# Optimization experiments

Hardware: AMD Instinct MI355X
Metric: run time of the kernel (lower is better)

Reference implementation:

```python
import jax, jax.numpy as jnp
import numpy as np

BETA = 0.25          # commitment loss weight (init kwarg)
CODEBOOK_SIZE = 2048


def setup_inputs() -> dict:
    key = jax.random.key(0)
    k1, k2 = jax.random.split(key)
    B, L, D = 8, 4096, 256
    z_e = jax.random.normal(k1, (B, L, D), dtype=jnp.float32)
    # xavier_uniform-style init for the codebook
    limit = float(np.sqrt(6.0 / (CODEBOOK_SIZE + D)))
    embed_weight = jax.random.uniform(k2, (CODEBOOK_SIZE, D), dtype=jnp.float32,
                                      minval=-limit, maxval=limit)
    return {"z_e": z_e, "embed_weight": embed_weight}


def reference(z_e, embed_weight):
    # eval-mode forward (no EMA buffer updates)
    B, L, D = z_e.shape
    K = embed_weight.shape[0]
    zf = z_e.reshape(-1, D)                                   # [N, D]
    d2 = (jnp.sum(zf * zf, axis=1, keepdims=True)
          - 2.0 * (zf @ embed_weight.T)
          + jnp.sum(embed_weight * embed_weight, axis=1)[None, :])
    distances = jnp.sqrt(jnp.maximum(d2, 0.0))                # [N, K]
    idx = jnp.argmin(distances, axis=1)                       # [N]
    z_q = embed_weight[idx].reshape(B, L, D)                  # gather

    commitment_loss = BETA * jnp.mean((jax.lax.stop_gradient(z_q) - z_e) ** 2)
    embedding_loss = jnp.mean((jax.lax.stop_gradient(z_e) - z_q) ** 2)

    # avg over one-hot encodings == normalized histogram of idx
    N = zf.shape[0]
    counts = jax.ops.segment_sum(jnp.ones((N,), jnp.float32), idx, num_segments=K)
    avg_probs = counts / N
    perplexity = jnp.exp(-jnp.sum(avg_probs * jnp.log(avg_probs + 1e-10)))
    vq_loss = commitment_loss + embedding_loss - 0.01 * perplexity

    z_q_st = z_e + jax.lax.stop_gradient(z_q - z_e)           # straight-through
    return z_q_st, vq_loss, idx.reshape(B, L)
```

## Files before the change

### kernel.cpp

```cpp
#include <hip/hip_runtime.h>
#include <math.h>

#define DDIM 256
#define NSPLIT 2
#define TILES_PER_SPLIT 32
#define TILE_CODES 32
#define TILE_BYTES 16384
#define ROWS_PER_BLOCK 128

typedef __attribute__((ext_vector_type(8))) short short8v;
typedef __attribute__((ext_vector_type(4))) float float4v;
typedef unsigned int u32;
typedef unsigned short u16;

__device__ __forceinline__ short f2bf(float x) {
    u32 u = __float_as_uint(x);
    u = u + 0x7fffu + ((u >> 16) & 1u);
    return (short)(u >> 16);
}

__device__ __forceinline__ float np_sq_chain(const float* v, int lane) {
    #pragma clang fp contract(off)
    const int half = lane >> 3, j = lane & 7;
    const float* base = v + half * 128 + j;
    float x = base[0];
    float c = x * x;
    #pragma unroll
    for (int m = 1; m < 16; ++m) {
        float y = base[8 * m];
        float s = y * y;
        c = c + s;
    }
    return c;
}

__device__ __forceinline__ float np_combine16(const float* c) {
    #pragma clang fp contract(off)
    float L = ((c[0] + c[1]) + (c[2] + c[3])) + ((c[4] + c[5]) + (c[6] + c[7]));
    float R = ((c[8] + c[9]) + (c[10] + c[11])) + ((c[12] + c[13]) + (c[14] + c[15]));
    return L + R;
}

__device__ __forceinline__ void ins3(float m, int k,
                                     float& v0, float& v1, float& v2,
                                     int& i0, int& i1, int& i2) {
    if (m < v0)      { v2 = v1; i2 = i1; v1 = v0; i1 = i0; v0 = m; i0 = k; }
    else if (m < v1) { v2 = v1; i2 = i1; v1 = m;  i1 = k; }
    else if (m < v2) { v2 = m;  i2 = k; }
}

__global__ void code_norms_np_kernel(const float* __restrict__ e, float* __restrict__ e2,
                                     int* __restrict__ counts) {
    __shared__ float buf[DDIM];
    __shared__ float ch[16];
    int k = blockIdx.x;
    int t = threadIdx.x;
    if (t == 0) counts[k] = 0;
    float4 v = *(const float4*)&e[(size_t)k * DDIM + t * 4];
    *(float4*)&buf[t * 4] = v;
    __syncthreads();
    if (t < 16) ch[t] = np_sq_chain(buf, t);
    __syncthreads();
    if (t == 0) e2[k] = np_combine16(ch);
}

__global__ void convert_permute_e_kernel(const float* __restrict__ e, char* __restrict__ ebf_p) {
    int id = blockIdx.x * 256 + threadIdx.x;
    int k = id >> 5, d8 = id & 31;
    const float* s = &e[(size_t)k * DDIM + d8 * 8];
    float4 f0 = *(const float4*)s;
    float4 f1 = *(const float4*)(s + 4);
    short8v v;
    v[0] = f2bf(f0.x); v[1] = f2bf(f0.y); v[2] = f2bf(f0.z); v[3] = f2bf(f0.w);
    v[4] = f2bf(f1.x); v[5] = f2bf(f1.y); v[6] = f2bf(f1.z); v[7] = f2bf(f1.w);
    *(short8v*)(ebf_p + ((size_t)(k >> 5) << 14) + d8 * 512 + (k & 31) * 16) = v;
}

__global__ __attribute__((amdgpu_flat_work_group_size(512, 512)))
void vq_cand_kernel(const float* __restrict__ z, const char* __restrict__ ebf_p,
                    const float* __restrict__ e2, float* __restrict__ cand_v,
                    u16* __restrict__ cand_i, int N) {
    __shared__ float e2s[1024];
    const int t    = threadIdx.x;
    const int w    = t >> 6;
    const int lane = t & 63;
    const int quad = lane >> 4;
    const int l15  = lane & 15;
    const int s    = blockIdx.y;
    const int rw   = blockIdx.x * ROWS_PER_BLOCK + w * 16;

    e2s[t]       = e2[s * 1024 + t];
    e2s[t + 512] = e2[s * 1024 + 512 + t];

    short8v zf[8];
    {
        const float* zr = &z[(size_t)(rw + l15) * DDIM];
        #pragma unroll
        for (int kk = 0; kk < 8; ++kk) {
            int d0 = kk * 32 + quad * 8;
            float4 f0 = *(const float4*)&zr[d0];
            float4 f1 = *(const float4*)&zr[d0 + 4];
            short8v v;
            v[0] = f2bf(f0.x); v[1] = f2bf(f0.y); v[2] = f2bf(f0.z); v[3] = f2bf(f0.w);
            v[4] = f2bf(f1.x); v[5] = f2bf(f1.y); v[6] = f2bf(f1.z); v[7] = f2bf(f1.w);
            zf[kk] = v;
        }
    }

    __syncthreads();

    float v0 = 3.4e38f, v1 = 3.4e38f, v2 = 3.4e38f;
    int   i0 = 0x7fff,  i1 = 0x7fff,  i2 = 0x7fff;

    const char* sbase = ebf_p + (size_t)s * TILES_PER_SPLIT * TILE_BYTES
                      + quad * 512 + l15 * 16;

    #pragma unroll 1
    for (int tt = 0; tt < TILES_PER_SPLIT; ++tt) {
        const char* tg = sbase + (size_t)tt * TILE_BYTES;

        float4v acc0 = (float4v)0.0f, acc1 = (float4v)0.0f;

        #pragma unroll
        for (int kk = 0; kk < 8; ++kk) {
            short8v a0 = *(const short8v*)(tg + kk * 2048);
            short8v a1 = *(const short8v*)(tg + kk * 2048 + 256);
            acc0 = __builtin_amdgcn_mfma_f32_16x16x32_bf16(a0, zf[kk], acc0, 0, 0, 0);
            acc1 = __builtin_amdgcn_mfma_f32_16x16x32_bf16(a1, zf[kk], acc1, 0, 0, 0);
        }

        const int kloc  = tt * TILE_CODES;
        const int kbase = s * 1024 + kloc;
        float4 e2a = *(const float4*)&e2s[kloc + quad * 4];
        float4 e2b = *(const float4*)&e2s[kloc + 16 + quad * 4];
        float m;
        m = fmaf(-2.0f, acc0[0], e2a.x); ins3(m, kbase + quad * 4 + 0,      v0, v1, v2, i0, i1, i2);
        m = fmaf(-2.0f, acc1[0], e2b.x); ins3(m, kbase + 16 + quad * 4 + 0, v0, v1, v2, i0, i1, i2);
        m = fmaf(-2.0f, acc0[1], e2a.y); ins3(m, kbase + quad * 4 + 1,      v0, v1, v2, i0, i1, i2);
        m = fmaf(-2.0f, acc1[1], e2b.y); ins3(m, kbase + 16 + quad * 4 + 1, v0, v1, v2, i0, i1, i2);
        m = fmaf(-2.0f, acc0[2], e2a.z); ins3(m, kbase + quad * 4 + 2,      v0, v1, v2, i0, i1, i2);
        m = fmaf(-2.0f, acc1[2], e2b.z); ins3(m, kbase + 16 + quad * 4 + 2, v0, v1, v2, i0, i1, i2);
        m = fmaf(-2.0f, acc0[3], e2a.w); ins3(m, kbase + quad * 4 + 3,      v0, v1, v2, i0, i1, i2);
        m = fmaf(-2.0f, acc1[3], e2b.w); ins3(m, kbase + 16 + quad * 4 + 3, v0, v1, v2, i0, i1, i2);
    }

    {
        float bm0 = 3.4e38f, bm1 = 3.4e38f, bm2 = 3.4e38f;
        int   bk0 = 0x7fff,  bk1 = 0x7fff,  bk2 = 0x7fff;
        #pragma unroll
        for (int q = 0; q < 4; ++q) {
            int src = l15 + q * 16;
            float m0 = __shfl(v0, src); int k0 = __shfl(i0, src);
            float m1 = __shfl(v1, src); int k1 = __shfl(i1, src);
            float m2 = __shfl(v2, src); int k2 = __shfl(i2, src);
            ins3(m0, k0, bm0, bm1, bm2, bk0, bk1, bk2);
            ins3(m1, k1, bm0, bm1, bm2, bk0, bk1, bk2);
            ins3(m2, k2, bm0, bm1, bm2, bk0, bk1, bk2);
        }
        if (quad == 0) {
            size_t base = ((size_t)s * N + (rw + l15)) * 3;
            cand_v[base]     = bm0;  cand_i[base]     = (u16)bk0;
            cand_v[base + 1] = bm1;  cand_i[base + 1] = (u16)bk1;
            cand_v[base + 2] = bm2;  cand_i[base + 2] = (u16)bk2;
        }
    }
}

__global__ void refine_fused_kernel(const float* __restrict__ z, const float* __restrict__ e,
                                    const float* __restrict__ e2np,
                                    const float* __restrict__ cand_v,
                                    const u16* __restrict__ cand_i,
                                    int* __restrict__ counts, float* __restrict__ partials,
                                    float* __restrict__ out_zq, float* __restrict__ out_idx,
                                    int N) {
    __shared__ float buf[4][DDIM];
    __shared__ float ch[4][16];
    __shared__ float wsum[4];
    const int w = threadIdx.x >> 6;
    const int t = threadIdx.x & 63;
    const int n = blockIdx.x * 4 + w;

    float4 zv = *(const float4*)&z[(size_t)n * DDIM + t * 4];
    *(float4*)&buf[w][t * 4] = zv;
    __syncthreads();
    if (t < 16) ch[w][t] = np_sq_chain(buf[w], t);
    __syncthreads();

    float bv[6]; int bi[6];
    #pragma unroll
    for (int c = 0; c < 6; ++c) { bv[c] = 3.4e38f; bi[c] = 0x7fffffff; }
    #pragma unroll
    for (int c = 0; c < 6; ++c) {
        int sp = c / 3, j = c - sp * 3;
        size_t off = ((size_t)sp * N + n) * 3 + j;
        float v  = cand_v[off];
        int   id = (int)cand_i[off];
        #pragma unroll
        for (int x = 0; x < 6; ++x) {
            if (v < bv[x] || (v == bv[x] && id < bi[x])) {
                for (int d = 5; d > x; --d) { bv[d] = bv[d - 1]; bi[d] = bi[d - 1]; }
                bv[x] = v; bi[x] = id;
                break;
            }
        }
    }

    float dotf[6];
    #pragma unroll
    for (int c = 0; c < 6; ++c) {
        int k = bi[c];
        float4 ev = *(const float4*)&e[(size_t)k * DDIM + t * 4];
        double p = (double)zv.x * (double)ev.x + (double)zv.y * (double)ev.y
                 + (double)zv.z * (double)ev.z + (double)zv.w * (double)ev.w;
        #pragma unroll
        for (int o = 32; o > 0; o >>= 1) p += __shfl_down(p, o);
        dotf[c] = (float)p;
    }

    int bk = 0;
    if (t == 0) {
        #pragma clang fp contract(off)
        float sx = np_combine16(ch[w]);
        float bd = 3.4e38f;
        bk = 0x7fffffff;
        #pragma unroll
        for (int c = 0; c < 6; ++c) {
            float twod = 2.0f * dotf[c];
            float t1 = sx - twod;
            float d2v = t1 + e2np[bi[c]];
            d2v = fmaxf(d2v, 0.0f);
            float d = sqrtf(d2v);
            if (d < bd || (d == bd && bi[c] < bk)) { bd = d; bk = bi[c]; }
        }
    }
    int wk = __shfl(bk, 0);

    float4 ev = *(const float4*)&e[(size_t)wk * DDIM + t * 4];
    *(float4*)&out_zq[(size_t)n * DDIM + t * 4] = ev;
    float dx = zv.x - ev.x, dy = zv.y - ev.y, dz = zv.z - ev.z, dw = zv.w - ev.w;
    float sq = dx * dx + dy * dy + dz * dz + dw * dw;
    #pragma unroll
    for (int o = 32; o > 0; o >>= 1) sq += __shfl_down(sq, o);
    if (t == 0) {
        wsum[w] = sq;
        atomicAdd(&counts[wk], 1);
        out_idx[n] = (float)wk;
    }
    __syncthreads();
    if (threadIdx.x == 0)
        partials[blockIdx.x] = wsum[0] + wsum[1] + wsum[2] + wsum[3];
}

__global__ void finalize_kernel(const int* __restrict__ counts, const float* __restrict__ partials,
                                float* __restrict__ out_loss, int K, int NB,
                                float invN, float invND) {
    int t = threadIdx.x;
    double ent = 0.0, sq = 0.0;
    for (int k = t; k < K; k += 256) {
        float p = (float)counts[k] * invN;
        ent += (double)(p * logf(p + 1e-10f));
    }
    for (int i = t; i < NB; i += 256) sq += (double)partials[i];
    #pragma unroll
    for (int o = 32; o > 0; o >>= 1) {
        ent += __shfl_down(ent, o);
        sq  += __shfl_down(sq, o);
    }
    __shared__ double e4[4], s4[4];
    if ((t & 63) == 0) { e4[t >> 6] = ent; s4[t >> 6] = sq; }
    __syncthreads();
    if (t == 0) {
        double esum = e4[0] + e4[1] + e4[2] + e4[3];
        double ssum = s4[0] + s4[1] + s4[2] + s4[3];
        float perp = expf((float)(-esum));
        float mean = (float)ssum * invND;
        out_loss[0] = 1.25f * mean - 0.01f * perp;
    }
}

extern "C" void kernel_launch(void* const* d_in, const int* in_sizes, int n_in,
                              void* d_out, int out_size, void* d_ws, size_t ws_size,
                              hipStream_t stream) {
    const float* z = (const float*)d_in[0];
    const float* e = (const float*)d_in[1];
    const int N = in_sizes[0] / DDIM;
    const int K = in_sizes[1] / DDIM;

    float* out      = (float*)d_out;
    float* out_zq   = out;
    float* out_loss = out + (size_t)N * DDIM;
    float* out_idx  = out_loss + 1;

    int*   counts   = (int*)d_ws;
    float* e2np     = (float*)((char*)d_ws + 8192);
    float* partials = (float*)((char*)d_ws + 16384);
    float* cand_v   = (float*)((char*)d_ws + 49152);
    u16*   cand_i   = (u16*)((char*)d_ws + 835584);
    char*  ebf_p    = (char*)d_ws + 1228800;

    code_norms_np_kernel<<<K, 64, 0, stream>>>(e, e2np, counts);
    convert_permute_e_kernel<<<K * 32 / 256, 256, 0, stream>>>(e, ebf_p);
    vq_cand_kernel<<<dim3(N / ROWS_PER_BLOCK, NSPLIT), 512, 0, stream>>>(z, ebf_p, e2np,
                                                                         cand_v, cand_i, N);
    refine_fused_kernel<<<N / 4, 256, 0, stream>>>(z, e, e2np, cand_v, cand_i,
                                                   counts, partials, out_zq, out_idx, N);
    finalize_kernel<<<1, 256, 0, stream>>>(counts, partials, out_loss, K, N / 4,
                                           1.0f / (float)N, 1.0f / (float)(N * DDIM));
}
```

Baseline: 404.4 us.

## Stage codebook panels in LDS with double-buffered async loads and 2x4 MFMA tiles

The candidate-search kernel now converts a block's 128 z rows to bf16 into LDS and streams 64-code codebook panels into a double-buffered LDS area using global_load_lds, instead of having every wave read the codebook straight from global memory. Each of the 4 waves computes a 32-row by 64-code tile (8 MFMAs per k-step), so each A and B fragment is reused twice or four times. The aim is to cut redundant global and L2 traffic for the codebook and overlap its loads with MFMA work. In exchange it uses about 100KB of LDS and 256 threads, which limits the GPU to one block per CU and depends on vmcnt-based waits for correctness.

```diff
diff --git a/kernel.cpp b/kernel.cpp
--- a/kernel.cpp
+++ b/kernel.cpp
@@ -3,9 +3,11 @@
 
 #define DDIM 256
 #define NSPLIT 2
-#define TILES_PER_SPLIT 32
-#define TILE_CODES 32
-#define TILE_BYTES 16384
+#define SPLIT_CODES 1024
+#define SPLIT_BYTES (SPLIT_CODES * DDIM * 2)
+#define PANEL_CODES 64
+#define PANELS_PER_SPLIT 16
+#define PANEL_BYTES 32768
 #define ROWS_PER_BLOCK 128
 
 typedef __attribute__((ext_vector_type(8))) short short8v;
@@ -17,6 +19,12 @@
     u32 u = __float_as_uint(x);
     u = u + 0x7fffu + ((u >> 16) & 1u);
     return (short)(u >> 16);
+}
+
+__device__ __forceinline__ void gload_lds16(const void* g, void* l) {
+    __builtin_amdgcn_global_load_lds(
+        (const __attribute__((address_space(1))) u32*)g,
+        (__attribute__((address_space(3))) u32*)l, 16, 0, 0);
 }
 
 __device__ __forceinline__ float np_sq_chain(const float* v, int lane) {
@@ -76,10 +84,12 @@
     *(short8v*)(ebf_p + ((size_t)(k >> 5) << 14) + d8 * 512 + (k & 31) * 16) = v;
 }
 
-__global__ __attribute__((amdgpu_flat_work_group_size(512, 512)))
+__global__ __launch_bounds__(256, 1)
 void vq_cand_kernel(const float* __restrict__ z, const char* __restrict__ ebf_p,
                     const float* __restrict__ e2, float* __restrict__ cand_v,
                     u16* __restrict__ cand_i, int N) {
+    __shared__ __align__(16) char cpan[2][PANEL_BYTES];
+    __shared__ __align__(16) char zlds[65536];
     __shared__ float e2s[1024];
     const int t    = threadIdx.x;
     const int w    = t >> 6;
@@ -87,83 +97,138 @@
     const int quad = lane >> 4;
     const int l15  = lane & 15;
     const int s    = blockIdx.y;
-    const int rw   = blockIdx.x * ROWS_PER_BLOCK + w * 16;
-
+    const int rw0  = blockIdx.x * ROWS_PER_BLOCK;
+
+    const char* cbase = ebf_p + (size_t)s * SPLIT_BYTES;
+
+    #pragma unroll
+    for (int i = 0; i < 16; ++i) {
+        int u = t + i * 256;
+        int row = u >> 5, c = u & 31;
+        const float* src = &z[(size_t)(rw0 + row) * DDIM + c * 8];
+        float4 f0 = *(const float4*)src;
+        float4 f1 = *(const float4*)(src + 4);
+        short8v v;
+        v[0] = f2bf(f0.x); v[1] = f2bf(f0.y); v[2] = f2bf(f0.z); v[3] = f2bf(f0.w);
+        v[4] = f2bf(f1.x); v[5] = f2bf(f1.y); v[6] = f2bf(f1.z); v[7] = f2bf(f1.w);
+        *(short8v*)(zlds + (row >> 4) * 8192 + c * 256 + (row & 15) * 16) = v;
+    }
     e2s[t]       = e2[s * 1024 + t];
+    e2s[t + 256] = e2[s * 1024 + 256 + t];
     e2s[t + 512] = e2[s * 1024 + 512 + t];
-
-    short8v zf[8];
-    {
-        const float* zr = &z[(size_t)(rw + l15) * DDIM];
+    e2s[t + 768] = e2[s * 1024 + 768 + t];
+
+#define STAGE_PANEL(P, BUF)                                                  \
+    {                                                                        \
+        const char* sp_ = cbase + (size_t)(P) * PANEL_BYTES;                 \
+        char* dp_ = cpan[BUF];                                               \
+        _Pragma("unroll")                                                    \
+        for (int j = 0; j < 8; ++j)                                          \
+            gload_lds16(sp_ + j * 4096 + t * 16, dp_ + j * 4096 + t * 16);   \
+    }
+    STAGE_PANEL(0, 0)
+    STAGE_PANEL(1, 1)
+
+    asm volatile("s_waitcnt lgkmcnt(0)" ::: "memory");
+    __builtin_amdgcn_s_barrier();
+
+    float tv00 = 3.4e38f, tv01 = 3.4e38f, tv02 = 3.4e38f;
+    int   ti00 = 0x7fff,  ti01 = 0x7fff,  ti02 = 0x7fff;
+    float tv10 = 3.4e38f, tv11 = 3.4e38f, tv12 = 3.4e38f;
+    int   ti10 = 0x7fff,  ti11 = 0x7fff,  ti12 = 0x7fff;
+
+    const char* zq = zlds + w * 16384 + quad * 256 + l15 * 16;
+
+    #pragma unroll 1
+    for (int p = 0; p < PANELS_PER_SPLIT; ++p) {
+        if (p < PANELS_PER_SPLIT - 1)
+            asm volatile("s_waitcnt vmcnt(8)" ::: "memory");
+        else
+            asm volatile("s_waitcnt vmcnt(0)" ::: "memory");
+        __builtin_amdgcn_s_barrier();
+
+        const char* es = cpan[p & 1];
+        const char* aq = es + quad * 512 + l15 * 16;
+
+        float4v c00 = (float4v)0.0f, c01 = (float4v)0.0f,
+                c02 = (float4v)0.0f, c03 = (float4v)0.0f;
+        float4v c10 = (float4v)0.0f, c11 = (float4v)0.0f,
+                c12 = (float4v)0.0f, c13 = (float4v)0.0f;
+
         #pragma unroll
         for (int kk = 0; kk < 8; ++kk) {
-            int d0 = kk * 32 + quad * 8;
-            float4 f0 = *(const float4*)&zr[d0];
-            float4 f1 = *(const float4*)&zr[d0 + 4];
-            short8v v;
-            v[0] = f2bf(f0.x); v[1] = f2bf(f0.y); v[2] = f2bf(f0.z); v[3] = f2bf(f0.w);
-            v[4] = f2bf(f1.x); v[5] = f2bf(f1.y); v[6] = f2bf(f1.z); v[7] = f2bf(f1.w);
-            zf[kk] = v;
+            const char* ak = aq + kk * 2048;
+            const char* zk = zq + kk * 1024;
+            short8v A0 = *(const short8v*)(ak);
+            short8v A1 = *(const short8v*)(ak + 256);
+            short8v A2 = *(const short8v*)(ak + 16384);
+            short8v A3 = *(const short8v*)(ak + 16384 + 256);
+            short8v B0 = *(const short8v*)(zk);
+            short8v B1 = *(const short8v*)(zk + 8192);
+            c00 = __builtin_amdgcn_mfma_f32_16x16x32_bf16(A0, B0, c00, 0, 0, 0);
+            c01 = __builtin_amdgcn_mfma_f32_16x16x32_bf16(A1, B0, c01, 0, 0, 0);
+            c02 = __builtin_amdgcn_mfma_f32_16x16x32_bf16(A2, B0, c02, 0, 0, 0);
+            c03 = __builtin_amdgcn_mfma_f32_16x16x32_bf16(A3, B0, c03, 0, 0, 0);
+            c10 = __builtin_amdgcn_mfma_f32_16x16x32_bf16(A0, B1, c10, 0, 0, 0);
+            c11 = __builtin_amdgcn_mfma_f32_16x16x32_bf16(A1, B1, c11, 0, 0, 0);
+            c12 = __builtin_amdgcn_mfma_f32_16x16x32_bf16(A2, B1, c12, 0, 0, 0);
+            c13 = __builtin_amdgcn_mfma_f32_16x16x32_bf16(A3, B1, c13, 0, 0, 0);
         }
-    }
-
-    __syncthreads();
-
-    float v0 = 3.4e38f, v1 = 3.4e38f, v2 = 3.4e38f;
-    int   i0 = 0x7fff,  i1 = 0x7fff,  i2 = 0x7fff;
-
-    const char* sbase = ebf_p + (size_t)s * TILES_PER_SPLIT * TILE_BYTES
-                      + quad * 512 + l15 * 16;
-
-    #pragma unroll 1
-    for (int tt = 0; tt < TILES_PER_SPLIT; ++tt) {
-        const char* tg = sbase + (size_t)tt * TILE_BYTES;
-
-        float4v acc0 = (float4v)0.0f, acc1 = (float4v)0.0f;
-
-        #pragma unroll
-        for (int kk = 0; kk < 8; ++kk) {
-            short8v a0 = *(const short8v*)(tg + kk * 2048);
-            short8v a1 = *(const short8v*)(tg + kk * 2048 + 256);
-            acc0 = __builtin_amdgcn_mfma_f32_16x16x32_bf16(a0, zf[kk], acc0, 0, 0, 0);
-            acc1 = __builtin_amdgcn_mfma_f32_16x16x32_bf16(a1, zf[kk], acc1, 0, 0, 0);
+
+        const int pb = p * PANEL_CODES;
+        const int kb = s * SPLIT_CODES + pb;
+#define FOLD4(ACC, EOFF, V0, V1, V2, I0, I1, I2)                             \
+        {                                                                    \
+            float4 E = *(const float4*)&e2s[pb + (EOFF) + quad * 4];         \
+            float mm;                                                        \
+            mm = fmaf(-2.0f, ACC[0], E.x); ins3(mm, kb + (EOFF) + quad * 4 + 0, V0, V1, V2, I0, I1, I2); \
+            mm = fmaf(-2.0f, ACC[1], E.y); ins3(mm, kb + (EOFF) + quad * 4 + 1, V0, V1, V2, I0, I1, I2); \
+            mm = fmaf(-2.0f, ACC[2], E.z); ins3(mm, kb + (EOFF) + quad * 4 + 2, V0, V1, V2, I0, I1, I2); \
+            mm = fmaf(-2.0f, ACC[3], E.w); ins3(mm, kb + (EOFF) + quad * 4 + 3, V0, V1, V2, I0, I1, I2); \
         }
-
-        const int kloc  = tt * TILE_CODES;
-        const int kbase = s * 1024 + kloc;
-        float4 e2a = *(const float4*)&e2s[kloc + quad * 4];
-        float4 e2b = *(const float4*)&e2s[kloc + 16 + quad * 4];
-        float m;
-        m = fmaf(-2.0f, acc0[0], e2a.x); ins3(m, kbase + quad * 4 + 0,      v0, v1, v2, i0, i1, i2);
-        m = fmaf(-2.0f, acc1[0], e2b.x); ins3(m, kbase + 16 + quad * 4 + 0, v0, v1, v2, i0, i1, i2);
-        m = fmaf(-2.0f, acc0[1], e2a.y); ins3(m, kbase + quad * 4 + 1,      v0, v1, v2, i0, i1, i2);
-        m = fmaf(-2.0f, acc1[1], e2b.y); ins3(m, kbase + 16 + quad * 4 + 1, v0, v1, v2, i0, i1, i2);
-        m = fmaf(-2.0f, acc0[2], e2a.z); ins3(m, kbase + quad * 4 + 2,      v0, v1, v2, i0, i1, i2);
-        m = fmaf(-2.0f, acc1[2], e2b.z); ins3(m, kbase + 16 + quad * 4 + 2, v0, v1, v2, i0, i1, i2);
-        m = fmaf(-2.0f, acc0[3], e2a.w); ins3(m, kbase + quad * 4 + 3,      v0, v1, v2, i0, i1, i2);
-        m = fmaf(-2.0f, acc1[3], e2b.w); ins3(m, kbase + 16 + quad * 4 + 3, v0, v1, v2, i0, i1, i2);
-    }
-
-    {
-        float bm0 = 3.4e38f, bm1 = 3.4e38f, bm2 = 3.4e38f;
-        int   bk0 = 0x7fff,  bk1 = 0x7fff,  bk2 = 0x7fff;
-        #pragma unroll
-        for (int q = 0; q < 4; ++q) {
-            int src = l15 + q * 16;
-            float m0 = __shfl(v0, src); int k0 = __shfl(i0, src);
-            float m1 = __shfl(v1, src); int k1 = __shfl(i1, src);
-            float m2 = __shfl(v2, src); int k2 = __shfl(i2, src);
-            ins3(m0, k0, bm0, bm1, bm2, bk0, bk1, bk2);
-            ins3(m1, k1, bm0, bm1, bm2, bk0, bk1, bk2);
-            ins3(m2, k2, bm0, bm1, bm2, bk0, bk1, bk2);
-        }
-        if (quad == 0) {
-            size_t base = ((size_t)s * N + (rw + l15)) * 3;
-            cand_v[base]     = bm0;  cand_i[base]     = (u16)bk0;
-            cand_v[base + 1] = bm1;  cand_i[base + 1] = (u16)bk1;
-            cand_v[base + 2] = bm2;  cand_i[base + 2] = (u16)bk2;
-        }
-    }
+        FOLD4(c00,  0, tv00, tv01, tv02, ti00, ti01, ti02)
+        FOLD4(c01, 16, tv00, tv01, tv02, ti00, ti01, ti02)
+        FOLD4(c02, 32, tv00, tv01, tv02, ti00, ti01, ti02)
+        FOLD4(c03, 48, tv00, tv01, tv02, ti00, ti01, ti02)
+        FOLD4(c10,  0, tv10, tv11, tv12, ti10, ti11, ti12)
+        FOLD4(c11, 16, tv10, tv11, tv12, ti10, ti11, ti12)
+        FOLD4(c12, 32, tv10, tv11, tv12, ti10, ti11, ti12)
+        FOLD4(c13, 48, tv10, tv11, tv12, ti10, ti11, ti12)
+#undef FOLD4
+
+        asm volatile("s_waitcnt lgkmcnt(0)" ::: "memory");
+        __builtin_amdgcn_s_barrier();
+
+        if (p + 2 < PANELS_PER_SPLIT)
+            STAGE_PANEL(p + 2, p & 1)
+    }
+#undef STAGE_PANEL
+
+#define MERGE_STORE(V0, V1, V2, I0, I1, I2, MOFF)                            \
+    {                                                                        \
+        float bm0 = 3.4e38f, bm1 = 3.4e38f, bm2 = 3.4e38f;                   \
+        int   bk0 = 0x7fff,  bk1 = 0x7fff,  bk2 = 0x7fff;                    \
+        _Pragma("unroll")                                                    \
+        for (int q = 0; q < 4; ++q) {                                        \
+            int src = l15 + q * 16;                                          \
+            float m0 = __shfl(V0, src); int k0 = __shfl(I0, src);            \
+            float m1 = __shfl(V1, src); int k1 = __shfl(I1, src);            \
+            float m2 = __shfl(V2, src); int k2 = __shfl(I2, src);            \
+            ins3(m0, k0, bm0, bm1, bm2, bk0, bk1, bk2);                      \
+            ins3(m1, k1, bm0, bm1, bm2, bk0, bk1, bk2);                      \
+            ins3(m2, k2, bm0, bm1, bm2, bk0, bk1, bk2);                      \
+        }                                                                    \
+        if (quad == 0) {                                                     \
+            int row = rw0 + w * 32 + (MOFF) + l15;                           \
+            size_t base = ((size_t)s * N + row) * 3;                         \
+            cand_v[base]     = bm0;  cand_i[base]     = (u16)bk0;            \
+            cand_v[base + 1] = bm1;  cand_i[base + 1] = (u16)bk1;            \
+            cand_v[base + 2] = bm2;  cand_i[base + 2] = (u16)bk2;            \
+        }                                                                    \
+    }
+    MERGE_STORE(tv00, tv01, tv02, ti00, ti01, ti02, 0)
+    MERGE_STORE(tv10, tv11, tv12, ti10, ti11, ti12, 16)
+#undef MERGE_STORE
 }
 
 __global__ void refine_fused_kernel(const float* __restrict__ z, const float* __restrict__ e,
@@ -300,7 +365,7 @@
 
     code_norms_np_kernel<<<K, 64, 0, stream>>>(e, e2np, counts);
     convert_permute_e_kernel<<<K * 32 / 256, 256, 0, stream>>>(e, ebf_p);
-    vq_cand_kernel<<<dim3(N / ROWS_PER_BLOCK, NSPLIT), 512, 0, stream>>>(z, ebf_p, e2np,
+    vq_cand_kernel<<<dim3(N / ROWS_PER_BLOCK, NSPLIT), 256, 0, stream>>>(z, ebf_p, e2np,
                                                                          cand_v, cand_i, N);
     refine_fused_kernel<<<N / 4, 256, 0, stream>>>(z, e, e2np, cand_v, cand_i,
                                                    counts, partials, out_zq, out_idx, N);
```

Measured after the change: 666.6 us. 64.8% more time.
